# Optimization experiments

Hardware: AMD Instinct MI355X
Metric: run time of the kernel (lower is better)

## Reference

```python
import jax, jax.numpy as jnp
import numpy as np

H = 70  # LSTM hidden size (hard-coded in module)

def _lstm_cell(x, h, c, Wih, Whh, bih, bhh):
    # torch gate order: i, f, g, o
    gates = x @ Wih.T + h @ Whh.T + bih + bhh  # [B, 4H]
    i, f, g, o = jnp.split(gates, 4, axis=-1)
    i = jax.nn.sigmoid(i); f = jax.nn.sigmoid(f)
    g = jnp.tanh(g);       o = jax.nn.sigmoid(o)
    c_new = f * c + i * g
    h_new = o * jnp.tanh(c_new)
    return h_new, c_new

def setup_inputs() -> dict:
    key = jax.random.key(0)
    ks = jax.random.split(key, 16)
    T, B, D = 512, 4096, 64
    s_in = 1.0 / np.sqrt(H)
    def u(k, shape):
        return jax.random.uniform(k, shape, jnp.float32, -s_in, s_in)
    return {
        "data_in": jax.random.normal(ks[0], (T, B, D), jnp.float32),
        "batch_dim": B,
        "W_ih0": u(ks[1], (4 * H, D)),  "W_hh0": u(ks[2], (4 * H, H)),
        "b_ih0": u(ks[3], (4 * H,)),    "b_hh0": u(ks[4], (4 * H,)),
        "W_ih1": u(ks[5], (4 * H, H)),  "W_hh1": u(ks[6], (4 * H, H)),
        "b_ih1": u(ks[7], (4 * H,)),    "b_hh1": u(ks[8], (4 * H,)),
        "W1": u(ks[9], (50, H)), "b1": u(ks[10], (50,)),
        "W2": u(ks[11], (1, 50)), "b2": u(ks[12], (1,)),
    }

def reference(data_in, batch_dim, W_ih0, W_hh0, b_ih0, b_hh0,
              W_ih1, W_hh1, b_ih1, b_hh1, W1, b1, W2, b2):
    B = data_in.shape[1]
    z = jnp.zeros((B, H), data_in.dtype)
    def step(carry, x_t):
        h0, c0, h1, c1 = carry
        h0, c0 = _lstm_cell(x_t, h0, c0, W_ih0, W_hh0, b_ih0, b_hh0)
        h1, c1 = _lstm_cell(h0, h1, c1, W_ih1, W_hh1, b_ih1, b_hh1)
        return (h0, c0, h1, c1), None
    (h0, c0, h1, c1), _ = jax.lax.scan(step, (z, z, z, z), data_in)
    # head uses h_n of the last (second) layer
    out = jax.nn.relu(h1 @ W1.T + b1)
    out = jax.nn.sigmoid(out @ W2.T + b2)  # [B, 1]
    return out
```

## Files before the change

### kernel.cpp

```cpp
#include <hip/hip_runtime.h>
#include <stdint.h>

#define T_STEPS 512
#define BATCH   4096
#define DIN     64
#define HID     70
#define KDIM    160
#define KS      5
#define RB      16
#define WAVES   12
#define NTHR    (WAVES*64)
#define NTILES  18
#define CH      3
#define ASP     232

typedef __bf16 bf16x8 __attribute__((ext_vector_type(8)));
typedef float  f32x4  __attribute__((ext_vector_type(4)));
typedef unsigned short ushort_t;
typedef ushort_t us4 __attribute__((ext_vector_type(4)));

#define NLOG2E   (-1.44269504088896340736f)
#define TWOLOG2E ( 2.88539008177792681472f)

__device__ __forceinline__ ushort_t f2bf(float f) {
    uint32_t u = __float_as_uint(f);
    u += 0x7fffu + ((u >> 16) & 1u);
    return (ushort_t)(u >> 16);
}
__device__ __forceinline__ float sigm(float x) {
    return __builtin_amdgcn_rcpf(1.0f + __expf(-x));
}

__device__ __forceinline__ float cell(const f32x4 a, float& cc) {
    float u0 = __builtin_amdgcn_exp2f(a[0]);
    float u1 = __builtin_amdgcn_exp2f(a[1]);
    float v  = __builtin_amdgcn_exp2f(fminf(a[2], 88.0f));
    float u3 = __builtin_amdgcn_exp2f(a[3]);
    float ig = (v - 1.0f) * __builtin_amdgcn_rcpf((1.0f + u0) * (1.0f + v));
    float f_ = __builtin_amdgcn_rcpf(1.0f + u1);
    float cn = fmaf(f_, cc, ig);
    cc = cn;
    float w  = __builtin_amdgcn_exp2f(fminf(cn * TWOLOG2E, 88.0f));
    return (w - 1.0f) * __builtin_amdgcn_rcpf((1.0f + u3) * (1.0f + w));
}

__global__ void prep_kernel(const float* __restrict__ Wih0, const float* __restrict__ Whh0,
                            const float* __restrict__ bih0, const float* __restrict__ bhh0,
                            const float* __restrict__ Wih1, const float* __restrict__ Whh1,
                            const float* __restrict__ bih1, const float* __restrict__ bhh1,
                            ushort_t* __restrict__ W0p, ushort_t* __restrict__ W1p,
                            float* __restrict__ B0p, float* __restrict__ B1p) {
    int idx = blockIdx.x * 256 + threadIdx.x;
    const int n = NTILES * 16 * KDIM;
    if (idx < n) {
        int row = idx / KDIM, k = idx - row * KDIM;
        int t = row >> 4, m = row & 15;
        int gate = m & 3, h = 4*t + (m >> 2);
        float sc = (gate == 2) ? TWOLOG2E : NLOG2E;
        float v0 = 0.f, v1 = 0.f;
        if (h < HID) {
            int g = gate * HID + h;
            if (k < 64)        v0 = Wih0[g*64 + k];
            else if (k < 134)  v0 = Whh0[g*HID + (k - 64)];
            if (k < 70)                   v1 = Wih1[g*HID + k];
            else if (k >= 80 && k < 150)  v1 = Whh1[g*HID + (k - 80)];
        }
        W0p[idx] = f2bf(sc * v0);
        W1p[idx] = f2bf(sc * v1);
    }
    if (idx < NTILES*16) {
        int t = idx >> 4, m = idx & 15;
        int gate = m & 3, h = 4*t + (m >> 2);
        float sc = (gate == 2) ? TWOLOG2E : NLOG2E;
        float s0 = 0.f, s1 = 0.f;
        if (h < HID) {
            int g = gate * HID + h;
            s0 = sc * (bih0[g] + bhh0[g]);
            s1 = sc * (bih1[g] + bhh1[g]);
        }
        B0p[idx] = s0; B1p[idx] = s1;
    }
}

__global__ __launch_bounds__(NTHR) void lstm_kernel(
    const float* __restrict__ x,
    const ushort_t* __restrict__ W0p, const ushort_t* __restrict__ W1p,
    const float* __restrict__ B0p, const float* __restrict__ B1p,
    const float* __restrict__ W1h, const float* __restrict__ b1h,
    const float* __restrict__ W2h, const float* __restrict__ b2h,
    float* __restrict__ out)
{
    __shared__ alignas(16) ushort_t P[2][RB*ASP];
    __shared__ float h1f[RB*HID];
    __shared__ float mid[RB*50];

    const int tid  = threadIdx.x;
    const int wave = tid >> 6;
    const int lane = tid & 63;
    const int n15  = lane & 15;
    const int q    = lane >> 4;
    const int blk  = blockIdx.x;
    const bool isL0 = (wave >= 6);
    const int lw   = isL0 ? wave - 6 : wave;
    const int t0   = lw * CH;

    const ushort_t* __restrict__ Wp = isL0 ? W0p : W1p;
    const float*    __restrict__ Bp = isL0 ? B0p : B1p;

    bf16x8 wA[CH][KS];
    f32x4  bias[CH];
    int    col[CH];
    #pragma unroll
    for (int c = 0; c < CH; c++) {
        const int rowb = ((t0 + c)*16 + n15)*KDIM + q*8;
        #pragma unroll
        for (int ks = 0; ks < KS; ks++)
            wA[c][ks] = *(const bf16x8*)(Wp + rowb + ks*32);
        bias[c] = *(const f32x4*)(Bp + (t0 + c)*16 + q*4);
        col[c]  = (t0 + c)*4 + q;
    }
    const int kbase = (isL0 ? 0 : 64) + n15*ASP + q*8;

    for (int i = tid; i < 2*RB*ASP; i += NTHR) (&P[0][0])[i] = 0;

    const int  xt   = tid - 384;
    const bool xl   = (xt >= 0) && (xt < 256);
    const int  xrow = xt >> 4;
    const int  xcol = (xt & 15) * 4;
    const float* xptr = x + ((size_t)blk*RB + xrow)*DIN + xcol;

    f32x4 x0v, x1v, xcur;
    if (xl) {
        x0v  = *(const f32x4*)(xptr);
        x1v  = *(const f32x4*)(xptr + (size_t)1*(BATCH*DIN));
        xcur = *(const f32x4*)(xptr + (size_t)2*(BATCH*DIN));
    }
    __syncthreads();
    if (xl) {
        us4 s0, s1;
        #pragma unroll
        for (int e = 0; e < 4; e++) { s0[e] = f2bf(x0v[e]); s1[e] = f2bf(x1v[e]); }
        *(us4*)(&P[1][xrow*ASP + xcol]) = s0;
        *(us4*)(&P[0][xrow*ASP + xcol]) = s1;
    }
    __syncthreads();

    float cc[CH] = {0.f, 0.f, 0.f};

    if (isL0) {
        bf16x8 b[KS];
        #pragma unroll
        for (int ks = 0; ks < KS; ks++)
            b[ks] = *(const bf16x8*)(&P[1][kbase + ks*32]);
        f32x4 acc[CH];
        #pragma unroll
        for (int c = 0; c < CH; c++) acc[c] = bias[c];
        #pragma unroll
        for (int ks = 0; ks < KS; ks++) {
            #pragma unroll
            for (int c = 0; c < CH; c++)
                acc[c] = __builtin_amdgcn_mfma_f32_16x16x32_bf16(wA[c][ks], b[ks], acc[c], 0,0,0);
        }
        #pragma unroll
        for (int c = 0; c < CH; c++) {
            float hv = cell(acc[c], cc[c]);
            P[0][n15*ASP + 64 + col[c]] = f2bf(hv);
        }
    }
    __syncthreads();

    for (int p = 0; p < T_STEPS; p++) {
        const int cur = p & 1, nxt = cur ^ 1;
        f32x4 xn;
        if (xl) {
            const int tn = (p+3 < T_STEPS) ? p+3 : T_STEPS-1;
            xn = *(const f32x4*)(xptr + (size_t)tn*(BATCH*DIN));
        }
        bf16x8 b[KS];
        #pragma unroll
        for (int ks = 0; ks < KS; ks++)
            b[ks] = *(const bf16x8*)(&P[cur][kbase + ks*32]);
        f32x4 acc[CH];
        #pragma unroll
        for (int c = 0; c < CH; c++) acc[c] = bias[c];
        #pragma unroll
        for (int ks = 0; ks < KS; ks++) {
            #pragma unroll
            for (int c = 0; c < CH; c++)
                acc[c] = __builtin_amdgcn_mfma_f32_16x16x32_bf16(wA[c][ks], b[ks], acc[c], 0,0,0);
        }
        if (xl) {
            us4 s;
            #pragma unroll
            for (int e = 0; e < 4; e++) s[e] = f2bf(xcur[e]);
            *(us4*)(&P[nxt][xrow*ASP + xcol]) = s;
        }
        #pragma unroll
        for (int c = 0; c < CH; c++) {
            float hv = cell(acc[c], cc[c]);
            ushort_t hb = f2bf(hv);
            if (isL0) {
                P[nxt][n15*ASP + 64 + col[c]] = hb;
            } else {
                P[nxt][n15*ASP + 144 + col[c]] = hb;
                if (p == T_STEPS-1 && col[c] < HID) h1f[n15*HID + col[c]] = hv;
            }
        }
        if (xl) xcur = xn;
        __syncthreads();
    }

    for (int uu = tid; uu < RB*50; uu += NTHR) {
        const int r = uu / 50, j = uu - r*50;
        float s = b1h[j];
        const float* wgt = W1h + j*HID;
        const float* hh  = h1f + r*HID;
        #pragma unroll 7
        for (int k = 0; k < HID; k++) s += wgt[k]*hh[k];
        mid[uu] = fmaxf(s, 0.0f);
    }
    __syncthreads();
    if (tid < RB) {
        float s = b2h[0];
        const float* m = mid + tid*50;
        #pragma unroll 10
        for (int j = 0; j < 50; j++) s += W2h[j]*m[j];
        out[blk*RB + tid] = sigm(s);
    }
}

extern "C" void kernel_launch(void* const* d_in, const int* in_sizes, int n_in,
                              void* d_out, int out_size, void* d_ws, size_t ws_size,
                              hipStream_t stream) {
    (void)in_sizes; (void)n_in; (void)out_size; (void)ws_size;
    const float* x    = (const float*)d_in[0];
    const float* Wih0 = (const float*)d_in[2];
    const float* Whh0 = (const float*)d_in[3];
    const float* bih0 = (const float*)d_in[4];
    const float* bhh0 = (const float*)d_in[5];
    const float* Wih1 = (const float*)d_in[6];
    const float* Whh1 = (const float*)d_in[7];
    const float* bih1 = (const float*)d_in[8];
    const float* bhh1 = (const float*)d_in[9];
    const float* W1h  = (const float*)d_in[10];
    const float* b1h  = (const float*)d_in[11];
    const float* W2h  = (const float*)d_in[12];
    const float* b2h  = (const float*)d_in[13];

    char* ws = (char*)d_ws;
    ushort_t* W0p = (ushort_t*)ws;
    ushort_t* W1p = (ushort_t*)(ws + 92160);
    float*    B0p = (float*)(ws + 184320);
    float*    B1p = (float*)(ws + 185472);

    prep_kernel<<<180, 256, 0, stream>>>(Wih0, Whh0, bih0, bhh0,
                                         Wih1, Whh1, bih1, bhh1,
                                         W0p, W1p, B0p, B1p);
    lstm_kernel<<<BATCH/RB, NTHR, 0, stream>>>(x, W0p, W1p, B0p, B1p,
                                               W1h, b1h, W2h, b2h, (float*)d_out);
}
```

Before: 1.037 ms.

## Split gate tiles across 16 waves and unroll step loop with packed bf16 converts

After: 1.054 ms. Within noise of the previous version (+1.6%).

```diff
diff --git a/kernel.cpp b/kernel.cpp
--- a/kernel.cpp
+++ b/kernel.cpp
@@ -8,16 +8,15 @@
 #define KDIM    160
 #define KS      5
 #define RB      16
-#define WAVES   12
+#define WAVES   16
 #define NTHR    (WAVES*64)
 #define NTILES  18
-#define CH      3
 #define ASP     232
+#define H1S     72
 
 typedef __bf16 bf16x8 __attribute__((ext_vector_type(8)));
 typedef float  f32x4  __attribute__((ext_vector_type(4)));
 typedef unsigned short ushort_t;
-typedef ushort_t us4 __attribute__((ext_vector_type(4)));
 
 #define NLOG2E   (-1.44269504088896340736f)
 #define TWOLOG2E ( 2.88539008177792681472f)
@@ -82,7 +81,7 @@
     }
 }
 
-__global__ __launch_bounds__(NTHR) void lstm_kernel(
+__global__ __launch_bounds__(NTHR, 4) void lstm_kernel(
     const float* __restrict__ x,
     const ushort_t* __restrict__ W0p, const ushort_t* __restrict__ W1p,
     const float* __restrict__ B0p, const float* __restrict__ B1p,
@@ -91,7 +90,7 @@
     float* __restrict__ out)
 {
     __shared__ alignas(16) ushort_t P[2][RB*ASP];
-    __shared__ float h1f[RB*HID];
+    __shared__ float h1f[RB*H1S];
     __shared__ float mid[RB*50];
 
     const int tid  = threadIdx.x;
@@ -100,32 +99,46 @@
     const int n15  = lane & 15;
     const int q    = lane >> 4;
     const int blk  = blockIdx.x;
-    const bool isL0 = (wave >= 6);
-    const int lw   = isL0 ? wave - 6 : wave;
-    const int t0   = lw * CH;
+    const bool isL0 = (wave & 1);
+    const int lw   = wave >> 1;
+    const bool cw3 = (lw < 2);
+    const int t0   = cw3 ? lw*3 : (6 + (lw-2)*2);
+    const int hcol0 = t0*4 + q;
 
     const ushort_t* __restrict__ Wp = isL0 ? W0p : W1p;
     const float*    __restrict__ Bp = isL0 ? B0p : B1p;
 
-    bf16x8 wA[CH][KS];
-    f32x4  bias[CH];
-    int    col[CH];
-    #pragma unroll
-    for (int c = 0; c < CH; c++) {
-        const int rowb = ((t0 + c)*16 + n15)*KDIM + q*8;
+    bf16x8 wA[3][KS];
+    f32x4  bias[3];
+    bias[2] = f32x4{0.f, 0.f, 0.f, 0.f};
+    {
+        const int r0 = (t0*16 + n15)*KDIM + q*8;
+        const int r1 = ((t0+1)*16 + n15)*KDIM + q*8;
         #pragma unroll
-        for (int ks = 0; ks < KS; ks++)
-            wA[c][ks] = *(const bf16x8*)(Wp + rowb + ks*32);
-        bias[c] = *(const f32x4*)(Bp + (t0 + c)*16 + q*4);
-        col[c]  = (t0 + c)*4 + q;
+        for (int ks = 0; ks < KS; ks++) {
+            wA[0][ks] = *(const bf16x8*)(Wp + r0 + ks*32);
+            wA[1][ks] = *(const bf16x8*)(Wp + r1 + ks*32);
+        }
+        bias[0] = *(const f32x4*)(Bp + t0*16 + q*4);
+        bias[1] = *(const f32x4*)(Bp + (t0+1)*16 + q*4);
+        if (cw3) {
+            const int r2 = ((t0+2)*16 + n15)*KDIM + q*8;
+            #pragma unroll
+            for (int ks = 0; ks < KS; ks++)
+                wA[2][ks] = *(const bf16x8*)(Wp + r2 + ks*32);
+            bias[2] = *(const f32x4*)(Bp + (t0+2)*16 + q*4);
+        }
     }
     const int kbase = (isL0 ? 0 : 64) + n15*ASP + q*8;
+    const int hoff  = isL0 ? 64 : 144;
+
+    float cc[3] = {0.f, 0.f, 0.f};
 
     for (int i = tid; i < 2*RB*ASP; i += NTHR) (&P[0][0])[i] = 0;
 
-    const int  xt   = tid - 384;
-    const bool xl   = (xt >= 0) && (xt < 256);
-    const int  xrow = xt >> 4;
+    const bool xl   = (wave >= 12);
+    const int  xt   = (wave - 12)*64 + lane;
+    const int  xrow = (xt >> 4) & 15;
     const int  xcol = (xt & 15) * 4;
     const float* xptr = x + ((size_t)blk*RB + xrow)*DIN + xcol;
 
@@ -137,84 +150,99 @@
     }
     __syncthreads();
     if (xl) {
-        us4 s0, s1;
-        #pragma unroll
-        for (int e = 0; e < 4; e++) { s0[e] = f2bf(x0v[e]); s1[e] = f2bf(x1v[e]); }
-        *(us4*)(&P[1][xrow*ASP + xcol]) = s0;
-        *(us4*)(&P[0][xrow*ASP + xcol]) = s1;
-    }
-    __syncthreads();
-
-    float cc[CH] = {0.f, 0.f, 0.f};
-
-    if (isL0) {
+        uint32_t a0, a1, b0, b1;
+        asm("v_cvt_pk_bf16_f32 %0, %1, %2" : "=v"(a0) : "v"(x0v[0]), "v"(x0v[1]));
+        asm("v_cvt_pk_bf16_f32 %0, %1, %2" : "=v"(a1) : "v"(x0v[2]), "v"(x0v[3]));
+        asm("v_cvt_pk_bf16_f32 %0, %1, %2" : "=v"(b0) : "v"(x1v[0]), "v"(x1v[1]));
+        asm("v_cvt_pk_bf16_f32 %0, %1, %2" : "=v"(b1) : "v"(x1v[2]), "v"(x1v[3]));
+        uint2 pa; pa.x = a0; pa.y = a1;
+        uint2 pb; pb.x = b0; pb.y = b1;
+        *(uint2*)(&P[1][xrow*ASP + xcol]) = pa;
+        *(uint2*)(&P[0][xrow*ASP + xcol]) = pb;
+    }
+    __syncthreads();
+
+    auto gemm = [&](const ushort_t* bp, float* hv) __attribute__((always_inline)) {
         bf16x8 b[KS];
         #pragma unroll
         for (int ks = 0; ks < KS; ks++)
-            b[ks] = *(const bf16x8*)(&P[1][kbase + ks*32]);
-        f32x4 acc[CH];
-        #pragma unroll
-        for (int c = 0; c < CH; c++) acc[c] = bias[c];
+            b[ks] = *(const bf16x8*)(bp + ks*32);
+        f32x4 a0 = bias[0], a1 = bias[1], a2 = bias[2];
         #pragma unroll
         for (int ks = 0; ks < KS; ks++) {
-            #pragma unroll
-            for (int c = 0; c < CH; c++)
-                acc[c] = __builtin_amdgcn_mfma_f32_16x16x32_bf16(wA[c][ks], b[ks], acc[c], 0,0,0);
-        }
-        #pragma unroll
-        for (int c = 0; c < CH; c++) {
-            float hv = cell(acc[c], cc[c]);
-            P[0][n15*ASP + 64 + col[c]] = f2bf(hv);
-        }
-    }
-    __syncthreads();
-
-    for (int p = 0; p < T_STEPS; p++) {
-        const int cur = p & 1, nxt = cur ^ 1;
+            a0 = __builtin_amdgcn_mfma_f32_16x16x32_bf16(wA[0][ks], b[ks], a0, 0,0,0);
+            a1 = __builtin_amdgcn_mfma_f32_16x16x32_bf16(wA[1][ks], b[ks], a1, 0,0,0);
+            if (cw3)
+                a2 = __builtin_amdgcn_mfma_f32_16x16x32_bf16(wA[2][ks], b[ks], a2, 0,0,0);
+        }
+        hv[0] = cell(a0, cc[0]);
+        hv[1] = cell(a1, cc[1]);
+        if (cw3) hv[2] = cell(a2, cc[2]);
+    };
+    auto storeh = [&](ushort_t* hp, const float* hv) __attribute__((always_inline)) {
+        uint32_t pk01;
+        asm("v_cvt_pk_bf16_f32 %0, %1, %2" : "=v"(pk01) : "v"(hv[0]), "v"(hv[1]));
+        hp[0] = (ushort_t)pk01;
+        hp[4] = (ushort_t)(pk01 >> 16);
+        if (cw3) {
+            uint32_t pk2;
+            asm("v_cvt_pk_bf16_f32 %0, %1, %2" : "=v"(pk2) : "v"(hv[2]), "v"(hv[2]));
+            hp[8] = (ushort_t)pk2;
+        }
+    };
+
+    if (isL0) {
+        float hv[3];
+        gemm(&P[1][kbase], hv);
+        storeh(&P[0][n15*ASP + 64 + hcol0], hv);
+    }
+    __syncthreads();
+
+    auto phase = [&](const int cur, const int p) __attribute__((always_inline)) {
+        const int nxt = cur ^ 1;
         f32x4 xn;
         if (xl) {
-            const int tn = (p+3 < T_STEPS) ? p+3 : T_STEPS-1;
+            int tn = p + 3; if (tn > T_STEPS-1) tn = T_STEPS-1;
             xn = *(const f32x4*)(xptr + (size_t)tn*(BATCH*DIN));
         }
-        bf16x8 b[KS];
-        #pragma unroll
-        for (int ks = 0; ks < KS; ks++)
-            b[ks] = *(const bf16x8*)(&P[cur][kbase + ks*32]);
-        f32x4 acc[CH];
-        #pragma unroll
-        for (int c = 0; c < CH; c++) acc[c] = bias[c];
-        #pragma unroll
-        for (int ks = 0; ks < KS; ks++) {
-            #pragma unroll
-            for (int c = 0; c < CH; c++)
-                acc[c] = __builtin_amdgcn_mfma_f32_16x16x32_bf16(wA[c][ks], b[ks], acc[c], 0,0,0);
-        }
+        float hv[3];
+        gemm(&P[cur][kbase], hv);
         if (xl) {
-            us4 s;
-            #pragma unroll
-            for (int e = 0; e < 4; e++) s[e] = f2bf(xcur[e]);
-            *(us4*)(&P[nxt][xrow*ASP + xcol]) = s;
-        }
-        #pragma unroll
-        for (int c = 0; c < CH; c++) {
-            float hv = cell(acc[c], cc[c]);
-            ushort_t hb = f2bf(hv);
-            if (isL0) {
-                P[nxt][n15*ASP + 64 + col[c]] = hb;
-            } else {
-                P[nxt][n15*ASP + 144 + col[c]] = hb;
-                if (p == T_STEPS-1 && col[c] < HID) h1f[n15*HID + col[c]] = hv;
-            }
-        }
-        if (xl) xcur = xn;
-        __syncthreads();
-    }
+            uint32_t s0, s1;
+            asm("v_cvt_pk_bf16_f32 %0, %1, %2" : "=v"(s0) : "v"(xcur[0]), "v"(xcur[1]));
+            asm("v_cvt_pk_bf16_f32 %0, %1, %2" : "=v"(s1) : "v"(xcur[2]), "v"(xcur[3]));
+            uint2 pv; pv.x = s0; pv.y = s1;
+            *(uint2*)(&P[nxt][xrow*ASP + xcol]) = pv;
+            xcur = xn;
+        }
+        storeh(&P[nxt][n15*ASP + hoff + hcol0], hv);
+        asm volatile("s_waitcnt lgkmcnt(0)" ::: "memory");
+        __builtin_amdgcn_s_barrier();
+        asm volatile("" ::: "memory");
+    };
+
+    #pragma unroll 1
+    for (int p = 0; p < T_STEPS - 2; p += 2) {
+        phase(0, p);
+        phase(1, p + 1);
+    }
+    phase(0, T_STEPS - 2);
+
+    if (!isL0) {
+        float hv[3];
+        gemm(&P[1][kbase], hv);
+        float* hd = &h1f[n15*H1S + hcol0];
+        hd[0] = hv[0];
+        hd[4] = hv[1];
+        if (cw3) hd[8] = hv[2];
+    }
+    __syncthreads();
 
     for (int uu = tid; uu < RB*50; uu += NTHR) {
         const int r = uu / 50, j = uu - r*50;
         float s = b1h[j];
         const float* wgt = W1h + j*HID;
-        const float* hh  = h1f + r*HID;
+        const float* hh  = h1f + r*H1S;
         #pragma unroll 7
         for (int k = 0; k < HID; k++) s += wgt[k]*hh[k];
         mid[uu] = fmaxf(s, 0.0f);
```
